# Kernel optimization log

Hardware: AMD Instinct MI355X
Metric: run time of the kernel (lower is better)

Reference implementation:

```python
import jax, jax.numpy as jnp
import numpy as np

N_PIXELS = 262144  # 512x512 FOV
N_COMP = 1000      # neuron components (columns of sparse A)
NNZ = 400000       # ~400 nonzero pixels per component
N_BG = 2           # dense background columns
BATCH = 128


def setup_inputs() -> dict:
    key = jax.random.key(0)
    k0, k1, k2, k3, k4 = jax.random.split(key, 5)
    X = jax.random.normal(k0, (BATCH, N_PIXELS), dtype=jnp.float32)
    A_rows = jax.random.randint(k1, (NNZ,), 0, N_PIXELS, dtype=jnp.int32)
    A_cols = jax.random.randint(k2, (NNZ,), 0, N_COMP, dtype=jnp.int32)
    A_vals = jax.random.normal(k3, (NNZ,), dtype=jnp.float32)
    b = jax.random.normal(k4, (N_PIXELS, N_BG), dtype=jnp.float32)
    n_AtA = jnp.float32(1000.0)  # Frobenius norm of Ab.T @ Ab (constant scalar)
    return {"X": X, "A_vals": A_vals, "b": b, "n_AtA": n_AtA,
            "A_rows": A_rows, "A_cols": A_cols}


def reference(X, A_vals, b, n_AtA, A_rows, A_cols):
    # Sparse A^T @ X^T in COO form: gather pixel rows of X, scale by values,
    # segment-sum into component rows. data: [nnz, batch]
    data = X[:, A_rows].T * A_vals[:, None]
    Y = jax.ops.segment_sum(data, A_cols, num_segments=N_COMP)  # [n_comp, batch]
    # Dense background term: b^T @ X^T -> [n_bg, batch]
    Y1 = jnp.einsum('pg,bp->gb', b, X)
    Y = jnp.concatenate([Y, Y1], axis=0) / n_AtA
    return Y
```

## Files before the change

### kernel.cpp

```cpp
#include <hip/hip_runtime.h>
#include <hip/hip_bf16.h>

typedef unsigned short u16;
typedef unsigned int   u32;

#define N_PIXELS 262144
#define N_COMP   1000
#define NNZ      400000
#define N_BG     2
#define BATCH    128

#define CAP        576
#define TP_PIX     32
#define TS         36
#define SC_BLOCKS  64
#define SC_EPB     (NNZ / SC_BLOCKS)
#define TP_BLOCKS  (N_PIXELS / TP_PIX)
#define HALF_MAX   ((CAP + 1) / 2)
#define BG_BLOCKS  256
#define BG_PPB     (N_PIXELS / BG_BLOCKS)

#define CNT_PAD 16

#define WS_CNT    0
#define WS_SLOTS  65536
#define WS_XT     (WS_SLOTS + (size_t)N_COMP * CAP * 8)
#define WS_NEED   (WS_XT + (size_t)N_PIXELS * BATCH * 2)

__device__ __forceinline__ float bflo(u32 w) { return __uint_as_float(w << 16); }
__device__ __forceinline__ float bfhi(u32 w) { return __uint_as_float(w & 0xffff0000u); }


__global__ __launch_bounds__(256, 8) void stage_kernel(
    const float* __restrict__ X,
    const int*   __restrict__ rows, const int* __restrict__ cols,
    const float* __restrict__ vals, const float* __restrict__ nAtA,
    int* __restrict__ cnts, int2* __restrict__ slots,
    u32* __restrict__ XT32)
{
    __shared__ float smem[BATCH * TS];
    const int tid = threadIdx.x;

    if (blockIdx.x < SC_BLOCKS) {
        int* hist = (int*)smem;
        int* base = hist + N_COMP;
        for (int i = tid; i < N_COMP; i += 256) hist[i] = 0;
        __syncthreads();

        const int e0 = blockIdx.x * SC_EPB;
        for (int j = e0 + tid; j < e0 + SC_EPB; j += 256)
            atomicAdd(&hist[cols[j]], 1);
        __syncthreads();

        for (int c = tid; c < N_COMP; c += 256) {
            const int n = hist[c];
            if (n) base[c] = atomicAdd(&cnts[c * CNT_PAD], n);
            hist[c] = 0;
        }
        __syncthreads();

        const float inv = 1.0f / nAtA[0];
        for (int j = e0 + tid; j < e0 + SC_EPB; j += 256) {
            const int c = cols[j];
            const int pos = base[c] + atomicAdd(&hist[c], 1);
            if (pos < CAP) {
                int2 e; e.x = rows[j]; e.y = __float_as_int(vals[j] * inv);
                slots[(size_t)c * CAP + pos] = e;
            }
        }
    } else {
        const int p0 = (blockIdx.x - SC_BLOCKS) * TP_PIX;
        const int k  = tid & 7;
        const int bq = tid >> 3;
#pragma unroll
        for (int pass = 0; pass < 4; ++pass) {
            const int b = pass * 32 + bq;
            const float4 x = *(const float4*)(X + (size_t)b * N_PIXELS + p0 + 4 * k);
            const int m = (b >> 4) & 7;
            *(float4*)&smem[b * TS + 4 * (k ^ m)] = x;
        }
        __syncthreads();

        const int p    = tid >> 3;
        const int j0   = (tid & 7) * 16;
        const int m    = (j0 >> 4) & 7;
        const int slot = 4 * ((p >> 2) ^ m) + (p & 3);
        const float* col = smem + slot;
        u32 out[8];
#pragma unroll
        for (int q = 0; q < 8; ++q) {
            const float lo = col[(j0 + 2 * q)     * TS];
            const float hi = col[(j0 + 2 * q + 1) * TS];
            __hip_bfloat162 h2 = __float22bfloat162_rn(make_float2(lo, hi));
            u32 w; __builtin_memcpy(&w, &h2, 4);
            out[q] = w;
        }
        uint4* dst = (uint4*)(XT32 + (size_t)(p0 + p) * 64 + (j0 >> 1));
        dst[0] = make_uint4(out[0], out[1], out[2], out[3]);
        dst[1] = make_uint4(out[4], out[5], out[6], out[7]);
    }
}


__global__ __launch_bounds__(256) void compute_kernel(
    const uint4* __restrict__ XP4,
    const int*   __restrict__ cnts,
    const int2*  __restrict__ slots,
    const float* __restrict__ bmat,
    const float* __restrict__ nAtA,
    float* __restrict__ Y)
{
    __shared__ char smem_raw[12544];
    const int tid  = threadIdx.x;
    const int wave = tid >> 6;
    const int lane = tid & 63;
    const int g    = tid >> 4;
    const int s    = tid & 15;
    const int blk  = blockIdx.x;

    if (blk < 2 * N_COMP) {
        const int comp = blk >> 1;
        const int half = blk & 1;

        int*   sro = (int*)smem_raw;
        float* svv = (float*)(sro + HALF_MAX);
        float* red = (float*)(svv + HALF_MAX);

        int cnt = cnts[comp * CNT_PAD]; if (cnt > CAP) cnt = CAP;
        const int n0  = (cnt + 1) >> 1;
        const int beg = half ? n0 : 0;
        const int n   = (half ? cnt : n0) - beg;
        const int n_pad = (n + 15) & ~15;

        const int2* sl = slots + (size_t)comp * CAP + beg;
        for (int i = tid; i < n_pad; i += 256) {
            int r = 0; float v = 0.0f;
            if (i < n) { const int2 e = sl[i]; r = e.x; v = __int_as_float(e.y); }
            sro[i] = r << 4;
            svv[i] = v;
        }
        __syncthreads();

        float acc[8] = {0, 0, 0, 0, 0, 0, 0, 0};
#pragma unroll 2
        for (int i = 0; i < n_pad; i += 16) {
            const int   e = i + g;
            const float v = svv[e];
            const uint4 x = XP4[sro[e] + s];
            acc[0] += v * bflo(x.x); acc[1] += v * bfhi(x.x);
            acc[2] += v * bflo(x.y); acc[3] += v * bfhi(x.y);
            acc[4] += v * bflo(x.z); acc[5] += v * bfhi(x.z);
            acc[6] += v * bflo(x.w); acc[7] += v * bfhi(x.w);
        }
#pragma unroll
        for (int m = 16; m <= 32; m <<= 1)
#pragma unroll
            for (int q = 0; q < 8; ++q) acc[q] += __shfl_xor(acc[q], m, 64);
        if (lane < 16)
#pragma unroll
            for (int q = 0; q < 8; ++q) red[wave * 128 + lane * 8 + q] = acc[q];
        __syncthreads();
        if (tid < 128) {
            const float r0 = red[tid] + red[128 + tid] + red[256 + tid] + red[384 + tid];
            atomicAdd(&Y[(size_t)comp * BATCH + tid], r0);
        }
    } else {
        float2* bb   = (float2*)smem_raw;
        float*  red0 = (float*)(bb + BG_PPB);
        float*  red1 = red0 + 512;

        const int p0 = (blk - 2 * N_COMP) * BG_PPB;
        const float2* bm2 = (const float2*)bmat;
        for (int i = tid; i < BG_PPB; i += 256) bb[i] = bm2[p0 + i];
        __syncthreads();

        float a0[8] = {0,0,0,0,0,0,0,0}, a1[8] = {0,0,0,0,0,0,0,0};
#pragma unroll 2
        for (int i = g; i < BG_PPB; i += 16) {
            const uint4  x  = XP4[(size_t)(p0 + i) * 16 + s];
            const float2 b2 = bb[i];
            const float f0 = bflo(x.x), f1 = bfhi(x.x), f2 = bflo(x.y), f3 = bfhi(x.y);
            const float f4 = bflo(x.z), f5 = bfhi(x.z), f6 = bflo(x.w), f7 = bfhi(x.w);
            a0[0] += b2.x * f0; a0[1] += b2.x * f1; a0[2] += b2.x * f2; a0[3] += b2.x * f3;
            a0[4] += b2.x * f4; a0[5] += b2.x * f5; a0[6] += b2.x * f6; a0[7] += b2.x * f7;
            a1[0] += b2.y * f0; a1[1] += b2.y * f1; a1[2] += b2.y * f2; a1[3] += b2.y * f3;
            a1[4] += b2.y * f4; a1[5] += b2.y * f5; a1[6] += b2.y * f6; a1[7] += b2.y * f7;
        }
#pragma unroll
        for (int m = 16; m <= 32; m <<= 1)
#pragma unroll
            for (int q = 0; q < 8; ++q) {
                a0[q] += __shfl_xor(a0[q], m, 64);
                a1[q] += __shfl_xor(a1[q], m, 64);
            }
        if (lane < 16)
#pragma unroll
            for (int q = 0; q < 8; ++q) {
                red0[wave * 128 + lane * 8 + q] = a0[q];
                red1[wave * 128 + lane * 8 + q] = a1[q];
            }
        __syncthreads();
        if (tid < 128) {
            const float inv = 1.0f / nAtA[0];
            float* Ybg = Y + (size_t)N_COMP * BATCH;
            const float r0 = red0[tid] + red0[128 + tid] + red0[256 + tid] + red0[384 + tid];
            const float r1 = red1[tid] + red1[128 + tid] + red1[256 + tid] + red1[384 + tid];
            atomicAdd(&Ybg[tid],         r0 * inv);
            atomicAdd(&Ybg[BATCH + tid], r1 * inv);
        }
    }
}


#define NB          8
#define NNZ_CHUNKS  64
#define CHUNK_SZ    ((NNZ + NNZ_CHUNKS - 1) / NNZ_CHUNKS)

__global__ __launch_bounds__(256) void fb_hist_kernel(
    const float* __restrict__ X, const float* __restrict__ vals,
    const int* __restrict__ rows, const int* __restrict__ cols,
    const float* __restrict__ nAtA, float* __restrict__ Y)
{
    __shared__ float hist[NB * N_COMP];
    const int tid = threadIdx.x, chunk = blockIdx.x, b0 = blockIdx.y * NB;
    for (int i = tid; i < NB * N_COMP; i += 256) hist[i] = 0.0f;
    __syncthreads();
    const float inv = 1.0f / nAtA[0];
    const int e0 = chunk * CHUNK_SZ;
    const int e1 = (e0 + CHUNK_SZ < NNZ) ? (e0 + CHUNK_SZ) : NNZ;
    const float* Xb = X + (size_t)b0 * N_PIXELS;
    for (int j = e0 + tid; j < e1; j += 256) {
        const int r = rows[j], c = cols[j];
        const float v = vals[j] * inv;
        float x[NB];
#pragma unroll
        for (int k = 0; k < NB; ++k) x[k] = Xb[(size_t)k * N_PIXELS + r];
#pragma unroll
        for (int k = 0; k < NB; ++k) atomicAdd(&hist[k * N_COMP + c], v * x[k]);
    }
    __syncthreads();
    for (int i = tid; i < N_COMP * NB; i += 256) {
        const int c = i >> 3, k = i & 7;
        atomicAdd(&Y[(size_t)c * BATCH + b0 + k], hist[k * N_COMP + c]);
    }
}

__global__ __launch_bounds__(256) void fb_bg_kernel(
    const float* __restrict__ X, const float* __restrict__ bmat,
    const float* __restrict__ nAtA, float* __restrict__ Y)
{
    const int b = blockIdx.x, chunk = blockIdx.y, tid = threadIdx.x;
    const int p0 = chunk * (N_PIXELS / 8);
    const float4* X4 = (const float4*)(X + (size_t)b * N_PIXELS + p0);
    const float4* B4 = (const float4*)(bmat + (size_t)p0 * N_BG);
    float s0 = 0.0f, s1 = 0.0f;
    for (int i = tid; i < (N_PIXELS / 8) / 4; i += 256) {
        const float4 x = X4[i];
        const float4 g0 = B4[2 * i], g1 = B4[2 * i + 1];
        s0 += x.x * g0.x + x.y * g0.z + x.z * g1.x + x.w * g1.z;
        s1 += x.x * g0.y + x.y * g0.w + x.z * g1.y + x.w * g1.w;
    }
#pragma unroll
    for (int off = 32; off > 0; off >>= 1) {
        s0 += __shfl_down(s0, off, 64);
        s1 += __shfl_down(s1, off, 64);
    }
    if ((tid & 63) == 0) {
        const float inv = 1.0f / nAtA[0];
        atomicAdd(&Y[(size_t)N_COMP * BATCH + b],       s0 * inv);
        atomicAdd(&Y[(size_t)(N_COMP + 1) * BATCH + b], s1 * inv);
    }
}


extern "C" void kernel_launch(void* const* d_in, const int* in_sizes, int n_in,
                              void* d_out, int out_size, void* d_ws, size_t ws_size,
                              hipStream_t stream) {
    const float* X     = (const float*)d_in[0];
    const float* Avals = (const float*)d_in[1];
    const float* bmat  = (const float*)d_in[2];
    const float* nAtA  = (const float*)d_in[3];
    const int*   Arows = (const int*)d_in[4];
    const int*   Acols = (const int*)d_in[5];
    float*       Y     = (float*)d_out;

    if (ws_size >= WS_NEED) {
        char* ws = (char*)d_ws;
        int*  cnts  = (int*)(ws + WS_CNT);
        int2* slots = (int2*)(ws + WS_SLOTS);
        u32*  XT32  = (u32*)(ws + WS_XT);

        hipMemsetAsync(cnts, 0, 65536, stream);
        hipMemsetAsync(d_out, 0, (size_t)out_size * sizeof(float), stream);

        stage_kernel<<<SC_BLOCKS + TP_BLOCKS, 256, 0, stream>>>(
            X, Arows, Acols, Avals, nAtA, cnts, slots, XT32);
        compute_kernel<<<2 * N_COMP + BG_BLOCKS, 256, 0, stream>>>(
            (const uint4*)XT32, cnts, slots, bmat, nAtA, Y);
    } else {
        hipMemsetAsync(d_out, 0, (size_t)out_size * sizeof(float), stream);
        dim3 sgrid(NNZ_CHUNKS, BATCH / NB);
        fb_hist_kernel<<<sgrid, 256, 0, stream>>>(X, Avals, Arows, Acols, nAtA, Y);
        dim3 bgrid(BATCH, 8);
        fb_bg_kernel<<<bgrid, 256, 0, stream>>>(X, bmat, nAtA, Y);
    }
}
```

Measured before the change: 270.5 us.

## Split COO bucketing into hist/scan/scatter kernels with deterministic per-block offsets

Replaces the fused stage kernel with separate kernels. A per-block histogram kernel and a wave-scan kernel compute exclusive offsets per (block, component). A scatter kernel then places entries, and the X transpose runs as its own kernel. The chunk count rises from 64 to 250 blocks so the bucketing work spreads over more CUs, and the global atomics and the cnts memset are removed. In exchange it adds three extra kernel launches and serializes the scatter with the transpose instead of overlapping them in one grid.

```diff
diff --git a/kernel.cpp b/kernel.cpp
--- a/kernel.cpp
+++ b/kernel.cpp
@@ -13,17 +13,16 @@
 #define CAP        576
 #define TP_PIX     32
 #define TS         36
-#define SC_BLOCKS  64
+#define TP_BLOCKS  (N_PIXELS / TP_PIX)
+#define SC_BLOCKS  250
 #define SC_EPB     (NNZ / SC_BLOCKS)
-#define TP_BLOCKS  (N_PIXELS / TP_PIX)
 #define HALF_MAX   ((CAP + 1) / 2)
 #define BG_BLOCKS  256
 #define BG_PPB     (N_PIXELS / BG_BLOCKS)
 
-#define CNT_PAD 16
-
 #define WS_CNT    0
-#define WS_SLOTS  65536
+#define WS_BCNT   4096
+#define WS_SLOTS  (WS_BCNT + SC_BLOCKS * N_COMP * 4)
 #define WS_XT     (WS_SLOTS + (size_t)N_COMP * CAP * 8)
 #define WS_NEED   (WS_XT + (size_t)N_PIXELS * BATCH * 2)
 
@@ -31,74 +30,104 @@
 __device__ __forceinline__ float bfhi(u32 w) { return __uint_as_float(w & 0xffff0000u); }
 
 
-__global__ __launch_bounds__(256, 8) void stage_kernel(
-    const float* __restrict__ X,
-    const int*   __restrict__ rows, const int* __restrict__ cols,
+__global__ __launch_bounds__(256) void hist_kernel(
+    const int* __restrict__ cols, int* __restrict__ bcnt)
+{
+    __shared__ int h[N_COMP];
+    const int tid = threadIdx.x;
+    for (int i = tid; i < N_COMP; i += 256) h[i] = 0;
+    __syncthreads();
+    const int e0 = blockIdx.x * SC_EPB;
+    for (int j = e0 + tid; j < e0 + SC_EPB; j += 256)
+        atomicAdd(&h[cols[j]], 1);
+    __syncthreads();
+    for (int i = tid; i < N_COMP; i += 256)
+        bcnt[blockIdx.x * N_COMP + i] = h[i];
+}
+
+__global__ __launch_bounds__(256) void scan_kernel(
+    int* __restrict__ bcnt, int* __restrict__ cnts)
+{
+    const int wave = threadIdx.x >> 6;
+    const int lane = threadIdx.x & 63;
+    const int c = blockIdx.x * 4 + wave;
+    int carry = 0;
+#pragma unroll
+    for (int ch = 0; ch < 4; ++ch) {
+        const int b = ch * 64 + lane;
+        int v = (b < SC_BLOCKS) ? bcnt[b * N_COMP + c] : 0;
+        int s = v;
+#pragma unroll
+        for (int off = 1; off < 64; off <<= 1) {
+            const int t = __shfl_up(s, off, 64);
+            if (lane >= off) s += t;
+        }
+        if (b < SC_BLOCKS) bcnt[b * N_COMP + c] = s - v + carry;
+        carry += __shfl(s, 63, 64);
+    }
+    if (lane == 0) cnts[c] = carry;
+}
+
+__global__ __launch_bounds__(256) void scatter_kernel(
+    const int* __restrict__ rows, const int* __restrict__ cols,
     const float* __restrict__ vals, const float* __restrict__ nAtA,
-    int* __restrict__ cnts, int2* __restrict__ slots,
-    u32* __restrict__ XT32)
+    const int* __restrict__ bcnt, int2* __restrict__ slots)
+{
+    __shared__ int sbase[N_COMP];
+    __shared__ int scur[N_COMP];
+    const int tid = threadIdx.x;
+    for (int i = tid; i < N_COMP; i += 256) {
+        sbase[i] = bcnt[blockIdx.x * N_COMP + i];
+        scur[i]  = 0;
+    }
+    __syncthreads();
+    const float inv = 1.0f / nAtA[0];
+    const int e0 = blockIdx.x * SC_EPB;
+    for (int j = e0 + tid; j < e0 + SC_EPB; j += 256) {
+        const int c   = cols[j];
+        const int pos = sbase[c] + atomicAdd(&scur[c], 1);
+        if (pos < CAP) {
+            int2 e; e.x = rows[j]; e.y = __float_as_int(vals[j] * inv);
+            slots[(size_t)c * CAP + pos] = e;
+        }
+    }
+}
+
+
+__global__ __launch_bounds__(256, 8) void transpose_kernel(
+    const float* __restrict__ X, u32* __restrict__ XT32)
 {
     __shared__ float smem[BATCH * TS];
     const int tid = threadIdx.x;
-
-    if (blockIdx.x < SC_BLOCKS) {
-        int* hist = (int*)smem;
-        int* base = hist + N_COMP;
-        for (int i = tid; i < N_COMP; i += 256) hist[i] = 0;
-        __syncthreads();
-
-        const int e0 = blockIdx.x * SC_EPB;
-        for (int j = e0 + tid; j < e0 + SC_EPB; j += 256)
-            atomicAdd(&hist[cols[j]], 1);
-        __syncthreads();
-
-        for (int c = tid; c < N_COMP; c += 256) {
-            const int n = hist[c];
-            if (n) base[c] = atomicAdd(&cnts[c * CNT_PAD], n);
-            hist[c] = 0;
-        }
-        __syncthreads();
-
-        const float inv = 1.0f / nAtA[0];
-        for (int j = e0 + tid; j < e0 + SC_EPB; j += 256) {
-            const int c = cols[j];
-            const int pos = base[c] + atomicAdd(&hist[c], 1);
-            if (pos < CAP) {
-                int2 e; e.x = rows[j]; e.y = __float_as_int(vals[j] * inv);
-                slots[(size_t)c * CAP + pos] = e;
-            }
-        }
-    } else {
-        const int p0 = (blockIdx.x - SC_BLOCKS) * TP_PIX;
-        const int k  = tid & 7;
-        const int bq = tid >> 3;
-#pragma unroll
-        for (int pass = 0; pass < 4; ++pass) {
-            const int b = pass * 32 + bq;
-            const float4 x = *(const float4*)(X + (size_t)b * N_PIXELS + p0 + 4 * k);
-            const int m = (b >> 4) & 7;
-            *(float4*)&smem[b * TS + 4 * (k ^ m)] = x;
-        }
-        __syncthreads();
-
-        const int p    = tid >> 3;
-        const int j0   = (tid & 7) * 16;
-        const int m    = (j0 >> 4) & 7;
-        const int slot = 4 * ((p >> 2) ^ m) + (p & 3);
-        const float* col = smem + slot;
-        u32 out[8];
-#pragma unroll
-        for (int q = 0; q < 8; ++q) {
-            const float lo = col[(j0 + 2 * q)     * TS];
-            const float hi = col[(j0 + 2 * q + 1) * TS];
-            __hip_bfloat162 h2 = __float22bfloat162_rn(make_float2(lo, hi));
-            u32 w; __builtin_memcpy(&w, &h2, 4);
-            out[q] = w;
-        }
-        uint4* dst = (uint4*)(XT32 + (size_t)(p0 + p) * 64 + (j0 >> 1));
-        dst[0] = make_uint4(out[0], out[1], out[2], out[3]);
-        dst[1] = make_uint4(out[4], out[5], out[6], out[7]);
-    }
+    const int p0  = blockIdx.x * TP_PIX;
+    const int k   = tid & 7;
+    const int bq  = tid >> 3;
+#pragma unroll
+    for (int pass = 0; pass < 4; ++pass) {
+        const int b = pass * 32 + bq;
+        const float4 x = *(const float4*)(X + (size_t)b * N_PIXELS + p0 + 4 * k);
+        const int m = (b >> 4) & 7;
+        *(float4*)&smem[b * TS + 4 * (k ^ m)] = x;
+    }
+    __syncthreads();
+
+    const int p    = tid >> 3;
+    const int j0   = (tid & 7) * 16;
+    const int m    = (j0 >> 4) & 7;
+    const int slot = 4 * ((p >> 2) ^ m) + (p & 3);
+    const float* col = smem + slot;
+    u32 out[8];
+#pragma unroll
+    for (int q = 0; q < 8; ++q) {
+        const float lo = col[(j0 + 2 * q)     * TS];
+        const float hi = col[(j0 + 2 * q + 1) * TS];
+        __hip_bfloat162 h2 = __float22bfloat162_rn(make_float2(lo, hi));
+        u32 w; __builtin_memcpy(&w, &h2, 4);
+        out[q] = w;
+    }
+    uint4* dst = (uint4*)(XT32 + (size_t)(p0 + p) * 64 + (j0 >> 1));
+    dst[0] = make_uint4(out[0], out[1], out[2], out[3]);
+    dst[1] = make_uint4(out[4], out[5], out[6], out[7]);
 }
 
 
@@ -126,7 +155,7 @@
         float* svv = (float*)(sro + HALF_MAX);
         float* red = (float*)(svv + HALF_MAX);
 
-        int cnt = cnts[comp * CNT_PAD]; if (cnt > CAP) cnt = CAP;
+        int cnt = cnts[comp]; if (cnt > CAP) cnt = CAP;
         const int n0  = (cnt + 1) >> 1;
         const int beg = half ? n0 : 0;
         const int n   = (half ? cnt : n0) - beg;
@@ -287,14 +316,17 @@
     if (ws_size >= WS_NEED) {
         char* ws = (char*)d_ws;
         int*  cnts  = (int*)(ws + WS_CNT);
+        int*  bcnt  = (int*)(ws + WS_BCNT);
         int2* slots = (int2*)(ws + WS_SLOTS);
         u32*  XT32  = (u32*)(ws + WS_XT);
 
-        hipMemsetAsync(cnts, 0, 65536, stream);
         hipMemsetAsync(d_out, 0, (size_t)out_size * sizeof(float), stream);
 
-        stage_kernel<<<SC_BLOCKS + TP_BLOCKS, 256, 0, stream>>>(
-            X, Arows, Acols, Avals, nAtA, cnts, slots, XT32);
+        hist_kernel<<<SC_BLOCKS, 256, 0, stream>>>(Acols, bcnt);
+        scan_kernel<<<SC_BLOCKS, 256, 0, stream>>>(bcnt, cnts);
+        scatter_kernel<<<SC_BLOCKS, 256, 0, stream>>>(
+            Arows, Acols, Avals, nAtA, bcnt, slots);
+        transpose_kernel<<<TP_BLOCKS, 256, 0, stream>>>(X, XT32);
         compute_kernel<<<2 * N_COMP + BG_BLOCKS, 256, 0, stream>>>(
             (const uint4*)XT32, cnts, slots, bmat, nAtA, Y);
     } else {
```

Result: no change. 274.7 us (+1.6%).

## Scatter COO entries with per-element global atomics and split components into quarters

Applied to the files above, without the earlier changes.

The staging scatter no longer uses 64 blocks with a shared-memory histogram and two passes. It now launches one thread per nonzero, and each thread claims its slot with a global atomic on the per-component counter. The compute kernel splits each component's entries across four blocks instead of two and drops the unroll pragma, so more blocks run in parallel and each block's serial gather loop is shorter. The cost is more global atomic contention on the counters, and twice as many atomicAdds into Y for the partial sums.

```diff
diff --git a/kernel.cpp b/kernel.cpp
--- a/kernel.cpp
+++ b/kernel.cpp
@@ -13,10 +13,9 @@
 #define CAP        576
 #define TP_PIX     32
 #define TS         36
-#define SC_BLOCKS  64
-#define SC_EPB     (NNZ / SC_BLOCKS)
 #define TP_BLOCKS  (N_PIXELS / TP_PIX)
-#define HALF_MAX   ((CAP + 1) / 2)
+#define SC_NB      ((NNZ + 255) / 256)
+#define QMAX       ((CAP + 3) / 4)
 #define BG_BLOCKS  256
 #define BG_PPB     (N_PIXELS / BG_BLOCKS)
 
@@ -31,7 +30,7 @@
 __device__ __forceinline__ float bfhi(u32 w) { return __uint_as_float(w & 0xffff0000u); }
 
 
-__global__ __launch_bounds__(256, 8) void stage_kernel(
+__global__ __launch_bounds__(256, 8) void pre_kernel(
     const float* __restrict__ X,
     const int*   __restrict__ rows, const int* __restrict__ cols,
     const float* __restrict__ vals, const float* __restrict__ nAtA,
@@ -41,35 +40,20 @@
     __shared__ float smem[BATCH * TS];
     const int tid = threadIdx.x;
 
-    if (blockIdx.x < SC_BLOCKS) {
-        int* hist = (int*)smem;
-        int* base = hist + N_COMP;
-        for (int i = tid; i < N_COMP; i += 256) hist[i] = 0;
-        __syncthreads();
-
-        const int e0 = blockIdx.x * SC_EPB;
-        for (int j = e0 + tid; j < e0 + SC_EPB; j += 256)
-            atomicAdd(&hist[cols[j]], 1);
-        __syncthreads();
-
-        for (int c = tid; c < N_COMP; c += 256) {
-            const int n = hist[c];
-            if (n) base[c] = atomicAdd(&cnts[c * CNT_PAD], n);
-            hist[c] = 0;
-        }
-        __syncthreads();
-
-        const float inv = 1.0f / nAtA[0];
-        for (int j = e0 + tid; j < e0 + SC_EPB; j += 256) {
-            const int c = cols[j];
-            const int pos = base[c] + atomicAdd(&hist[c], 1);
+    if (blockIdx.x < SC_NB) {
+        const int j = blockIdx.x * 256 + tid;
+        if (j < NNZ) {
+            const int c   = cols[j];
+            const int pos = atomicAdd(&cnts[c * CNT_PAD], 1);
             if (pos < CAP) {
-                int2 e; e.x = rows[j]; e.y = __float_as_int(vals[j] * inv);
+                int2 e;
+                e.x = rows[j];
+                e.y = __float_as_int(vals[j] * (1.0f / nAtA[0]));
                 slots[(size_t)c * CAP + pos] = e;
             }
         }
     } else {
-        const int p0 = (blockIdx.x - SC_BLOCKS) * TP_PIX;
+        const int p0 = (blockIdx.x - SC_NB) * TP_PIX;
         const int k  = tid & 7;
         const int bq = tid >> 3;
 #pragma unroll
@@ -118,18 +102,19 @@
     const int s    = tid & 15;
     const int blk  = blockIdx.x;
 
-    if (blk < 2 * N_COMP) {
-        const int comp = blk >> 1;
-        const int half = blk & 1;
+    if (blk < 4 * N_COMP) {
+        const int comp = blk >> 2;
+        const int qr   = blk & 3;
 
         int*   sro = (int*)smem_raw;
-        float* svv = (float*)(sro + HALF_MAX);
-        float* red = (float*)(svv + HALF_MAX);
+        float* svv = (float*)(sro + QMAX);
+        float* red = (float*)(svv + QMAX);
 
         int cnt = cnts[comp * CNT_PAD]; if (cnt > CAP) cnt = CAP;
-        const int n0  = (cnt + 1) >> 1;
-        const int beg = half ? n0 : 0;
-        const int n   = (half ? cnt : n0) - beg;
+        const int per = (cnt + 3) >> 2;
+        const int beg = qr * per;
+        int end = beg + per; if (end > cnt) end = cnt;
+        const int n = (end > beg) ? (end - beg) : 0;
         const int n_pad = (n + 15) & ~15;
 
         const int2* sl = slots + (size_t)comp * CAP + beg;
@@ -142,7 +127,6 @@
         __syncthreads();
 
         float acc[8] = {0, 0, 0, 0, 0, 0, 0, 0};
-#pragma unroll 2
         for (int i = 0; i < n_pad; i += 16) {
             const int   e = i + g;
             const float v = svv[e];
@@ -169,7 +153,7 @@
         float*  red0 = (float*)(bb + BG_PPB);
         float*  red1 = red0 + 512;
 
-        const int p0 = (blk - 2 * N_COMP) * BG_PPB;
+        const int p0 = (blk - 4 * N_COMP) * BG_PPB;
         const float2* bm2 = (const float2*)bmat;
         for (int i = tid; i < BG_PPB; i += 256) bb[i] = bm2[p0 + i];
         __syncthreads();
@@ -293,9 +277,9 @@
         hipMemsetAsync(cnts, 0, 65536, stream);
         hipMemsetAsync(d_out, 0, (size_t)out_size * sizeof(float), stream);
 
-        stage_kernel<<<SC_BLOCKS + TP_BLOCKS, 256, 0, stream>>>(
+        pre_kernel<<<SC_NB + TP_BLOCKS, 256, 0, stream>>>(
             X, Arows, Acols, Avals, nAtA, cnts, slots, XT32);
-        compute_kernel<<<2 * N_COMP + BG_BLOCKS, 256, 0, stream>>>(
+        compute_kernel<<<4 * N_COMP + BG_BLOCKS, 256, 0, stream>>>(
             (const uint4*)XT32, cnts, slots, bmat, nAtA, Y);
     } else {
         hipMemsetAsync(d_out, 0, (size_t)out_size * sizeof(float), stream);
```

Result: no change. 267.4 us (-1.1%).
